# Kernel optimization log

Hardware: AMD Instinct MI355X
Metric: run time of the kernel (lower is better)

## Reference

```python
import jax, jax.numpy as jnp
import numpy as np
from jax import lax

B_, L_, D_ = 4, 3136, 256
DH, DS, DR = 256, 16, 16  # d_inner//2, d_state, dt_rank (ceil(256/16))


def _ln(x, g, b):
    m = x.mean(-1, keepdims=True)
    v = ((x - m) ** 2).mean(-1, keepdims=True)
    return (x - m) * lax.rsqrt(v + 1e-5) * g + b


def _dwconv_same(x, w):
    # x: (B, C, L), w: (C, 1, K) depthwise, padding='same', no bias
    return lax.conv_general_dilated(x, w, (1,), 'SAME',
        dimension_numbers=('NCH', 'OIH', 'NCH'), feature_group_count=x.shape[1])


def _selective_scan(u, delta, A, Bm, Cm, Dp, delta_bias):
    # u, delta: (b, d, l); A: (d, n); Bm, Cm: (b, n, l)
    delta = jax.nn.softplus(delta + delta_bias[None, :, None])
    dA = jnp.exp(jnp.einsum('bdl,dn->lbdn', delta, A))          # (l,b,d,n)
    dBu = jnp.einsum('bdl,bnl,bdl->lbdn', delta, Bm, u)          # (l,b,d,n)
    C_l = jnp.transpose(Cm, (2, 0, 1))                           # (l,b,n)
    h0 = jnp.zeros(dA.shape[1:], u.dtype)

    def step(h, inp):
        dA_t, dBu_t, C_t = inp
        h = dA_t * h + dBu_t
        return h, jnp.einsum('bdn,bn->bd', h, C_t)

    _, ys = lax.scan(step, h0, (dA, dBu, C_l))                   # ys: (l,b,d)
    return jnp.transpose(ys, (1, 2, 0)) + u * Dp[None, :, None]


def _mamba(x, in_proj_w, conv_x_w, conv_z_w, x_proj_w, dt_proj_w, dt_proj_b, A_log, Dp, out_proj_w):
    xz = jnp.einsum('bld,ed->bel', x, in_proj_w)                 # (b, 2*DH, l)
    xb, zb = xz[:, :DH], xz[:, DH:]
    xb = jax.nn.silu(_dwconv_same(xb, conv_x_w))
    zb = jax.nn.silu(_dwconv_same(zb, conv_z_w))
    x_dbl = jnp.einsum('bdl,ed->ble', xb, x_proj_w)              # (b, l, DR+2*DS)
    dt, Bm, Cm = x_dbl[..., :DR], x_dbl[..., DR:DR + DS], x_dbl[..., DR + DS:]
    delta = jnp.einsum('blr,dr->bdl', dt, dt_proj_w)             # (b, DH, l)
    Bm = jnp.transpose(Bm, (0, 2, 1))                            # (b, DS, l)
    Cm = jnp.transpose(Cm, (0, 2, 1))
    A = -jnp.exp(A_log)
    y = _selective_scan(xb, delta, A, Bm, Cm, Dp, dt_proj_b)     # (b, DH, l)
    y = jnp.concatenate([y, zb], axis=1)                         # (b, 2*DH, l)
    return jnp.einsum('bel,de->bld', y, out_proj_w)


def _block(x, ln1_g, ln1_b, ln2_g, ln2_b, in_proj_w, conv_x_w, conv_z_w,
           x_proj_w, dt_proj_w, dt_proj_b, A_log, Dp, out_proj_w,
           mlp_w1, mlp_b1, mlp_w2, mlp_b2):
    x = x + _mamba(_ln(x, ln1_g, ln1_b), in_proj_w, conv_x_w, conv_z_w,
                   x_proj_w, dt_proj_w, dt_proj_b, A_log, Dp, out_proj_w)
    h = _ln(x, ln2_g, ln2_b)
    h = jax.nn.gelu(jnp.einsum('bld,hd->blh', h, mlp_w1) + mlp_b1, approximate=False)
    return x + (jnp.einsum('blh,dh->bld', h, mlp_w2) + mlp_b2)


def setup_inputs() -> dict:
    key = jax.random.key(0)
    ks = jax.random.split(key, 12)
    f = lambda k, s, sc=0.02: jax.random.normal(k, s, dtype=jnp.float32) * sc
    dt = jnp.exp(jax.random.uniform(ks[9], (DH,), dtype=jnp.float32)
                 * (np.log(0.1) - np.log(0.001)) + np.log(0.001))
    dt = jnp.clip(dt, 1e-4)
    inv_dt = dt + jnp.log(-jnp.expm1(-dt))
    return {
        'x': jax.random.normal(ks[0], (B_, L_, D_), dtype=jnp.float32),
        'ln1_g': jnp.ones((D_,), jnp.float32), 'ln1_b': jnp.zeros((D_,), jnp.float32),
        'ln2_g': jnp.ones((D_,), jnp.float32), 'ln2_b': jnp.zeros((D_,), jnp.float32),
        'in_proj_w': f(ks[1], (2 * DH, D_)),
        'conv_x_w': f(ks[2], (DH, 1, 3), 0.1),
        'conv_z_w': f(ks[3], (DH, 1, 3), 0.1),
        'x_proj_w': f(ks[4], (DR + 2 * DS, DH)),
        'dt_proj_w': f(ks[5], (DH, DR), DR ** -0.5),
        'dt_proj_b': inv_dt,
        'A_log': jnp.log(jnp.tile(jnp.arange(1, DS + 1, dtype=jnp.float32)[None, :], (DH, 1))),
        'Dp': jnp.ones((DH,), jnp.float32),
        'out_proj_w': f(ks[6], (D_, 2 * DH)),
        'mlp_w1': f(ks[7], (4 * D_, D_)), 'mlp_b1': jnp.zeros((4 * D_,), jnp.float32),
        'mlp_w2': f(ks[8], (D_, 4 * D_)), 'mlp_b2': jnp.zeros((D_,), jnp.float32),
    }


def reference(x, ln1_g, ln1_b, ln2_g, ln2_b, in_proj_w, conv_x_w, conv_z_w,
              x_proj_w, dt_proj_w, dt_proj_b, A_log, Dp, out_proj_w,
              mlp_w1, mlp_b1, mlp_w2, mlp_b2):
    return _block(x, ln1_g, ln1_b, ln2_g, ln2_b, in_proj_w, conv_x_w, conv_z_w,
                  x_proj_w, dt_proj_w, dt_proj_b, A_log, Dp, out_proj_w,
                  mlp_w1, mlp_b1, mlp_w2, mlp_b2)
```

## Files before the change

kernel.cpp:

```cpp
#include <hip/hip_runtime.h>
#include <hip/hip_bf16.h>

#define B_ 4
#define L_ 3136
#define D_ 256
#define NCH 49
#define LCH 64
#define M_ (B_*L_)

__device__ __forceinline__ float bf2f(unsigned short u) {
    union { unsigned int i; float f; } v; v.i = ((unsigned int)u) << 16; return v.f;
}
__device__ __forceinline__ unsigned short f2bs(float f) {
    __hip_bfloat16 h = __float2bfloat16(f);
    return *(unsigned short*)&h;
}
__device__ __forceinline__ float ldw(const void* p, size_t i, bool bf) {
    return bf ? bf2f(((const unsigned short*)p)[i]) : ((const float*)p)[i];
}
__device__ __forceinline__ void cvt4(ushort4 a, float* o) {
    o[0] = bf2f(a.x); o[1] = bf2f(a.y); o[2] = bf2f(a.z); o[3] = bf2f(a.w);
}
__device__ __forceinline__ void cvt8g(const unsigned short* p, bool v, float* o) {
    if (v) {
        ushort4 a = *(const ushort4*)p;
        ushort4 b = *(const ushort4*)(p + 4);
        cvt4(a, o); cvt4(b, o + 4);
    } else {
        #pragma unroll
        for (int i = 0; i < 8; ++i) o[i] = 0.f;
    }
}
__device__ __forceinline__ float dpp_add_xor1(float x) {
    int m = __builtin_amdgcn_update_dpp(0, __float_as_int(x), 0xB1, 0xF, 0xF, true);
    return x + __int_as_float(m);
}
__device__ __forceinline__ float dpp_add_xor2(float x) {
    int m = __builtin_amdgcn_update_dpp(0, __float_as_int(x), 0x4E, 0xF, 0xF, true);
    return x + __int_as_float(m);
}

__global__ __launch_bounds__(256) void detect_kernel(
    const unsigned int* __restrict__ xw, int* __restrict__ flag)
{
    int t = threadIdx.x; int cnt = 0;
    for (int i = t; i < 2048; i += 256) {
        unsigned int lo = xw[i] & 0xFFFFu;
        unsigned int e = (lo >> 7) & 0xFFu;
        if (e >= 0x58u && e <= 0x97u) cnt++;
    }
    #pragma unroll
    for (int o = 32; o > 0; o >>= 1) cnt += __shfl_down(cnt, o);
    __shared__ int sred[4];
    if ((t & 63) == 0) sred[t >> 6] = cnt;
    __syncthreads();
    if (t == 0) flag[0] = (sred[0] + sred[1] + sred[2] + sred[3] > 1024) ? 1 : 0;
}

__global__ __launch_bounds__(256) void ln_kernel(
    const void* __restrict__ xin, int inmode,
    const void* __restrict__ g, const void* __restrict__ bsh,
    unsigned short* __restrict__ out, const int* __restrict__ flagp)
{
    const bool wbf = (*flagp != 0);
    const bool inbf = (inmode < 0) ? wbf : true;
    int row = blockIdx.x * 4 + (threadIdx.x >> 6);
    int lane = threadIdx.x & 63;
    size_t idx = (size_t)row * 256 + lane * 4;
    float v[4];
    if (inbf) {
        ushort4 a = *(const ushort4*)((const unsigned short*)xin + idx);
        cvt4(a, v);
    } else {
        float4 a = *(const float4*)((const float*)xin + idx);
        v[0] = a.x; v[1] = a.y; v[2] = a.z; v[3] = a.w;
    }
    float s = v[0] + v[1] + v[2] + v[3];
    float s2 = v[0]*v[0] + v[1]*v[1] + v[2]*v[2] + v[3]*v[3];
    #pragma unroll
    for (int o = 32; o > 0; o >>= 1) { s += __shfl_xor(s, o); s2 += __shfl_xor(s2, o); }
    float mean = s * (1.f / 256.f);
    float var  = s2 * (1.f / 256.f) - mean * mean;
    float rs = rsqrtf(var + 1e-5f);
    ushort4 o;
    o.x = f2bs((v[0] - mean) * rs * ldw(g, lane*4+0, wbf) + ldw(bsh, lane*4+0, wbf));
    o.y = f2bs((v[1] - mean) * rs * ldw(g, lane*4+1, wbf) + ldw(bsh, lane*4+1, wbf));
    o.z = f2bs((v[2] - mean) * rs * ldw(g, lane*4+2, wbf) + ldw(bsh, lane*4+2, wbf));
    o.w = f2bs((v[3] - mean) * rs * ldw(g, lane*4+3, wbf) + ldw(bsh, lane*4+3, wbf));
    *(ushort4*)(out + idx) = o;
}

enum { EPI_NONE = 0, EPI_SP = 1, EPI_RES = 2, EPI_GELU = 3, EPI_OUT = 4 };

typedef __attribute__((ext_vector_type(8))) short bf16x8;
typedef __attribute__((ext_vector_type(4))) float f32x4;

__device__ __forceinline__ void gload_lds16(const void* g, void* l) {
    __builtin_amdgcn_global_load_lds(
        (const __attribute__((address_space(1))) unsigned int*)g,
        (__attribute__((address_space(3))) unsigned int*)l, 16, 0, 0);
}

template<int EPI>
__global__ __launch_bounds__(256) void mgemm_kernel(
    const unsigned short* __restrict__ A, const unsigned short* __restrict__ A2, int Ksplit,
    const void* __restrict__ W, void* __restrict__ Cout,
    int N, int K, int lda, int ldc,
    const void* __restrict__ bias, const void* __restrict__ resb,
    const unsigned short* __restrict__ resf, const int* __restrict__ flagp)
{
    const bool wbf = (*flagp != 0);
    __shared__ unsigned short As[2][64][64];
    __shared__ unsigned short Ws[2][64][64];
    const int tid = threadIdx.x;

    const int nwg = gridDim.x * gridDim.y;
    int bid = blockIdx.y * gridDim.x + blockIdx.x;
    int wgid = ((nwg & 7) == 0) ? ((bid & 7) * (nwg >> 3) + (bid >> 3)) : bid;
    const int bx = wgid % gridDim.x;
    const int by = wgid / gridDim.x;
    const int bm = by * 64, bn = bx * 64;

    const int l = tid & 63, wid = tid >> 6;
    const int wr = wid >> 1, wc = wid & 1;
    const int lr = l & 15;
    const int lq = l >> 4;
    const int srow = tid >> 3;
    const int sblk = ((tid & 7) ^ (srow & 7)) * 8;
    const int dcol = (tid & 7) * 8;

    f32x4 acc[2][2] = {};
    const int NT = K >> 6;

    auto stage = [&](int buf, int k0s) {
        const unsigned short* Ab; int kc;
        if (k0s < Ksplit) { Ab = A;  kc = k0s; }
        else              { Ab = A2; kc = k0s - Ksplit; }
        gload_lds16(Ab + (size_t)(bm + srow) * lda + kc + sblk,      &As[buf][srow][dcol]);
        gload_lds16(Ab + (size_t)(bm + 32 + srow) * lda + kc + sblk, &As[buf][32 + srow][dcol]);
        if (wbf) {
            const unsigned short* Wb = (const unsigned short*)W;
            gload_lds16(Wb + (size_t)(bn + srow) * K + k0s + sblk,      &Ws[buf][srow][dcol]);
            gload_lds16(Wb + (size_t)(bn + 32 + srow) * K + k0s + sblk, &Ws[buf][32 + srow][dcol]);
        } else {
            const float* Wf = (const float*)W;
            #pragma unroll
            for (int h = 0; h < 2; ++h) {
                int row = h * 32 + srow;
                const float* p = Wf + (size_t)(bn + row) * K + k0s + (tid & 7) * 8;
                float4 w0 = *(const float4*)p;
                float4 w1 = *(const float4*)(p + 4);
                ushort4 o0, o1;
                o0.x = f2bs(w0.x); o0.y = f2bs(w0.y); o0.z = f2bs(w0.z); o0.w = f2bs(w0.w);
                o1.x = f2bs(w1.x); o1.y = f2bs(w1.y); o1.z = f2bs(w1.z); o1.w = f2bs(w1.w);
                *(ushort4*)&Ws[buf][row][sblk]     = o0;
                *(ushort4*)&Ws[buf][row][sblk + 4] = o1;
            }
        }
    };

    stage(0, 0);
    asm volatile("s_waitcnt vmcnt(0)" ::: "memory");
    __syncthreads();

    int cur = 0;
    for (int kt = 0; kt < NT; ++kt) {
        if (kt + 1 < NT) stage(cur ^ 1, (kt + 1) << 6);

        bf16x8 af[2][2], bfr[2][2];
        #pragma unroll
        for (int i = 0; i < 2; ++i) {
            #pragma unroll
            for (int ks = 0; ks < 2; ++ks) {
                int ca = ((ks * 4 + lq) ^ (lr & 7)) * 8;
                af[i][ks]  = *(const bf16x8*)&As[cur][wr * 32 + i * 16 + lr][ca];
                bfr[i][ks] = *(const bf16x8*)&Ws[cur][wc * 32 + i * 16 + lr][ca];
            }
        }
        #pragma unroll
        for (int ks = 0; ks < 2; ++ks)
            #pragma unroll
            for (int i = 0; i < 2; ++i)
                #pragma unroll
                for (int j = 0; j < 2; ++j)
                    acc[i][j] = __builtin_amdgcn_mfma_f32_16x16x32_bf16(af[i][ks], bfr[j][ks], acc[i][j], 0, 0, 0);

        if (kt + 1 < NT) {
            asm volatile("s_waitcnt vmcnt(0)" ::: "memory");
            __syncthreads();
            cur ^= 1;
        }
    }

    #pragma unroll
    for (int i = 0; i < 2; ++i) {
        #pragma unroll
        for (int j = 0; j < 2; ++j) {
            const int col = bn + wc * 32 + j * 16 + lr;
            #pragma unroll
            for (int e = 0; e < 4; ++e) {
                const int row = bm + wr * 32 + i * 16 + lq * 4 + e;
                float t = acc[i][j][e];
                if (EPI == EPI_RES) {
                    t += ldw(resb, (size_t)row * 256 + col, wbf);
                } else if (EPI == EPI_GELU) {
                    t += ldw(bias, col, wbf);
                    t = 0.5f * t * (1.f + erff(t * 0.70710678118654752f));
                } else if (EPI == EPI_OUT) {
                    t += ldw(bias, col, wbf) + bf2f(resf[(size_t)row * 256 + col]);
                }
                if (EPI == EPI_OUT && !wbf) {
                    ((float*)Cout)[(size_t)row * ldc + col] = t;
                } else {
                    ((unsigned short*)Cout)[(size_t)row * ldc + col] = f2bs(t);
                }
            }
        }
    }
}

__global__ __launch_bounds__(256) void xproj_kernel(
    const unsigned short* __restrict__ A, const void* __restrict__ W,
    float* __restrict__ Cout, const int* __restrict__ flagp)
{
    const bool wbf = (*flagp != 0);
    __shared__ unsigned short As[2][64][64];
    __shared__ unsigned short Ws[2][64][64];
    const int tid = threadIdx.x;
    const int bm = blockIdx.y * 64;

    const int l = tid & 63, wid = tid >> 6;
    const int wr = wid >> 1, wc = wid & 1;
    const int lr = l & 15, lq = l >> 4;
    const int srow = tid >> 3;
    const int sblk = ((tid & 7) ^ (srow & 7)) * 8;
    const int dcol = (tid & 7) * 8;

    {
        ushort4 zz4; zz4.x = 0; zz4.y = 0; zz4.z = 0; zz4.w = 0;
        int buf = tid >> 7, rr = 48 + ((tid >> 3) & 15), cc = (tid & 7) * 8;
        *(ushort4*)&Ws[buf][rr][cc] = zz4;
        *(ushort4*)&Ws[buf][rr][cc + 4] = zz4;
    }
    __syncthreads();

    f32x4 acc[2][2] = {};

    auto stage = [&](int buf, int k0s) {
        gload_lds16(A + (size_t)(bm + srow) * 256 + k0s + sblk,      &As[buf][srow][dcol]);
        gload_lds16(A + (size_t)(bm + 32 + srow) * 256 + k0s + sblk, &As[buf][32 + srow][dcol]);
        if (wbf) {
            const unsigned short* Wb = (const unsigned short*)W;
            gload_lds16(Wb + (size_t)srow * 256 + k0s + sblk, &Ws[buf][srow][dcol]);
            if (srow < 16)
                gload_lds16(Wb + (size_t)(32 + srow) * 256 + k0s + sblk, &Ws[buf][32 + srow][dcol]);
        } else {
            const float* Wf = (const float*)W;
            #pragma unroll
            for (int h = 0; h < 2; ++h) {
                int row = h * 32 + srow;
                if (row < 48) {
                    const float* p = Wf + (size_t)row * 256 + k0s + (tid & 7) * 8;
                    float4 w0 = *(const float4*)p;
                    float4 w1 = *(const float4*)(p + 4);
                    ushort4 o0, o1;
                    o0.x = f2bs(w0.x); o0.y = f2bs(w0.y); o0.z = f2bs(w0.z); o0.w = f2bs(w0.w);
                    o1.x = f2bs(w1.x); o1.y = f2bs(w1.y); o1.z = f2bs(w1.z); o1.w = f2bs(w1.w);
                    *(ushort4*)&Ws[buf][row][sblk]     = o0;
                    *(ushort4*)&Ws[buf][row][sblk + 4] = o1;
                }
            }
        }
    };

    stage(0, 0);
    asm volatile("s_waitcnt vmcnt(0)" ::: "memory");
    __syncthreads();

    int cur = 0;
    for (int kt = 0; kt < 4; ++kt) {
        if (kt + 1 < 4) stage(cur ^ 1, (kt + 1) << 6);
        bf16x8 af[2][2], bfr[2][2];
        #pragma unroll
        for (int i = 0; i < 2; ++i) {
            #pragma unroll
            for (int ks = 0; ks < 2; ++ks) {
                int ca = ((ks * 4 + lq) ^ (lr & 7)) * 8;
                af[i][ks]  = *(const bf16x8*)&As[cur][wr * 32 + i * 16 + lr][ca];
                bfr[i][ks] = *(const bf16x8*)&Ws[cur][wc * 32 + i * 16 + lr][ca];
            }
        }
        #pragma unroll
        for (int ks = 0; ks < 2; ++ks)
            #pragma unroll
            for (int i = 0; i < 2; ++i)
                #pragma unroll
                for (int j = 0; j < 2; ++j)
                    acc[i][j] = __builtin_amdgcn_mfma_f32_16x16x32_bf16(af[i][ks], bfr[j][ks], acc[i][j], 0, 0, 0);
        if (kt + 1 < 4) {
            asm volatile("s_waitcnt vmcnt(0)" ::: "memory");
            __syncthreads();
            cur ^= 1;
        }
    }

    #pragma unroll
    for (int i = 0; i < 2; ++i) {
        #pragma unroll
        for (int j = 0; j < 2; ++j) {
            const int col = wc * 32 + j * 16 + lr;
            if (col < 48) {
                #pragma unroll
                for (int e = 0; e < 4; ++e) {
                    const int row = bm + wr * 32 + i * 16 + lq * 4 + e;
                    Cout[(size_t)row * 48 + col] = acc[i][j][e];
                }
            }
        }
    }
}

__global__ __launch_bounds__(256) void dtgemm_kernel(
    const float* __restrict__ Axd, const void* __restrict__ W,
    unsigned short* __restrict__ Cout, const void* __restrict__ bias,
    const int* __restrict__ flagp)
{
    const bool wbf = (*flagp != 0);
    __shared__ unsigned short Ah[64][16];
    __shared__ unsigned short Al[64][16];
    __shared__ unsigned short Wb[64][16];
    const int tid = threadIdx.x;
    const int nwg = gridDim.x * gridDim.y;
    int bid = blockIdx.y * gridDim.x + blockIdx.x;
    int wgid = ((nwg & 7) == 0) ? ((bid & 7) * (nwg >> 3) + (bid >> 3)) : bid;
    const int bx = wgid % gridDim.x, by = wgid / gridDim.x;
    const int bm = by * 64, bn = bx * 64;

    {
        int rr = tid >> 2, cc = (tid & 3) * 4;
        float4 v = *(const float4*)(Axd + (size_t)(bm + rr) * 48 + cc);
        float vv[4] = {v.x, v.y, v.z, v.w};
        ushort4 hi4, lo4;
        unsigned short* hp = (unsigned short*)&hi4;
        unsigned short* lp = (unsigned short*)&lo4;
        #pragma unroll
        for (int j = 0; j < 4; ++j) {
            unsigned short h = f2bs(vv[j]);
            hp[j] = h;
            lp[j] = f2bs(vv[j] - bf2f(h));
        }
        *(ushort4*)&Ah[rr][cc] = hi4;
        *(ushort4*)&Al[rr][cc] = lo4;
        ushort4 wb4;
        unsigned short* wp = (unsigned short*)&wb4;
        if (wbf) {
            wb4 = *(const ushort4*)((const unsigned short*)W + (size_t)(bn + rr) * 16 + cc);
        } else {
            float4 wv = *(const float4*)((const float*)W + (size_t)(bn + rr) * 16 + cc);
            wp[0] = f2bs(wv.x); wp[1] = f2bs(wv.y); wp[2] = f2bs(wv.z); wp[3] = f2bs(wv.w);
        }
        *(ushort4*)&Wb[rr][cc] = wb4;
    }
    __syncthreads();

    const int l = tid & 63, wid = tid >> 6;
    const int wr = wid >> 1, wc = wid & 1;
    const int lr = l & 15, lq = l >> 4;

    f32x4 acc[2][2] = {};
    bf16x8 ah[2], al8[2], wb8[2];
    #pragma unroll
    for (int i = 0; i < 2; ++i) { ah[i] = bf16x8{}; al8[i] = bf16x8{}; wb8[i] = bf16x8{}; }
    if (lq < 2) {
        #pragma unroll
        for (int i = 0; i < 2; ++i) {
            ah[i]  = *(const bf16x8*)&Ah[wr * 32 + i * 16 + lr][lq * 8];
            al8[i] = *(const bf16x8*)&Al[wr * 32 + i * 16 + lr][lq * 8];
            wb8[i] = *(const bf16x8*)&Wb[wc * 32 + i * 16 + lr][lq * 8];
        }
    }
    #pragma unroll
    for (int i = 0; i < 2; ++i)
        #pragma unroll
        for (int j = 0; j < 2; ++j) {
            acc[i][j] = __builtin_amdgcn_mfma_f32_16x16x32_bf16(ah[i],  wb8[j], acc[i][j], 0, 0, 0);
            acc[i][j] = __builtin_amdgcn_mfma_f32_16x16x32_bf16(al8[i], wb8[j], acc[i][j], 0, 0, 0);
        }

    #pragma unroll
    for (int i = 0; i < 2; ++i) {
        #pragma unroll
        for (int j = 0; j < 2; ++j) {
            const int col = bn + wc * 32 + j * 16 + lr;
            #pragma unroll
            for (int e = 0; e < 4; ++e) {
                const int row = bm + wr * 32 + i * 16 + lq * 4 + e;
                float t = acc[i][j][e] + ldw(bias, col, wbf);
                t = (t > 20.f) ? t : log1pf(__expf(t));
                Cout[(size_t)row * 256 + col] = f2bs(t);
            }
        }
    }
}

__global__ __launch_bounds__(256) void conv_silu_kernel(
    const unsigned short* __restrict__ xz,
    const void* __restrict__ wx, const void* __restrict__ wz,
    unsigned short* __restrict__ u, unsigned short* __restrict__ z,
    const int* __restrict__ flagp)
{
    const bool wbf = (*flagp != 0);
    int sub = threadIdx.x >> 5;
    int cb = (threadIdx.x & 31) * 8;
    int bl = blockIdx.x * 8 + sub;
    int l = bl % L_;
    const unsigned short* r = xz + (size_t)bl * 512;
    bool hasm = (l > 0), hasp = (l < L_ - 1);

    float wxa[24], wza[24];
    if (wbf) {
        const unsigned short* px = (const unsigned short*)wx + 3 * cb;
        const unsigned short* pz = (const unsigned short*)wz + 3 * cb;
        #pragma unroll
        for (int t = 0; t < 3; ++t) {
            cvt4(*(const ushort4*)(px + t * 8), &wxa[t * 8]);
            cvt4(*(const ushort4*)(px + t * 8 + 4), &wxa[t * 8 + 4]);
            cvt4(*(const ushort4*)(pz + t * 8), &wza[t * 8]);
            cvt4(*(const ushort4*)(pz + t * 8 + 4), &wza[t * 8 + 4]);
        }
    } else {
        const float* px = (const float*)wx + 3 * cb;
        const float* pz = (const float*)wz + 3 * cb;
        #pragma unroll
        for (int t = 0; t < 6; ++t) {
            *(float4*)&wxa[t * 4] = *(const float4*)(px + t * 4);
            *(float4*)&wza[t * 4] = *(const float4*)(pz + t * 4);
        }
    }

    float xm[8], xc[8], xp[8];
    cvt8g(r + cb - 512, hasm, xm);
    cvt8g(r + cb,       true, xc);
    cvt8g(r + cb + 512, hasp, xp);
    ushort4 o0, o1;
    {
        unsigned short* op = (unsigned short*)&o0;
        unsigned short* op1 = (unsigned short*)&o1;
        #pragma unroll
        for (int j = 0; j < 8; ++j) {
            float v = xm[j] * wxa[3 * j] + xc[j] * wxa[3 * j + 1] + xp[j] * wxa[3 * j + 2];
            v = v / (1.f + __expf(-v));
            if (j < 4) op[j] = f2bs(v); else op1[j - 4] = f2bs(v);
        }
    }
    *(ushort4*)(u + (size_t)bl * 256 + cb) = o0;
    *(ushort4*)(u + (size_t)bl * 256 + cb + 4) = o1;

    cvt8g(r + cb - 256,  hasm, xm);
    cvt8g(r + 256 + cb,  true, xc);
    cvt8g(r + 768 + cb,  hasp, xp);
    {
        unsigned short* op = (unsigned short*)&o0;
        unsigned short* op1 = (unsigned short*)&o1;
        #pragma unroll
        for (int j = 0; j < 8; ++j) {
            float v = xm[j] * wza[3 * j] + xc[j] * wza[3 * j + 1] + xp[j] * wza[3 * j + 2];
            v = v / (1.f + __expf(-v));
            if (j < 4) op[j] = f2bs(v); else op1[j - 4] = f2bs(v);
        }
    }
    *(ushort4*)(z + (size_t)bl * 256 + cb) = o0;
    *(ushort4*)(z + (size_t)bl * 256 + cb + 4) = o1;
}

__global__ __launch_bounds__(256) void scan_a_kernel(
    const unsigned short* __restrict__ delta, const unsigned short* __restrict__ u,
    const float* __restrict__ xdbl, const void* __restrict__ A_log,
    float* __restrict__ hend, float* __restrict__ dsum, const int* __restrict__ flagp)
{
    const bool wbf = (*flagp != 0);
    int blk = blockIdx.x;
    int b = blk / (NCH * 16);
    int rem = blk % (NCH * 16);
    int c = rem / 16, db = rem % 16;

    __shared__ unsigned int sdu[64][16];
    __shared__ float sB[64][16];

    const unsigned short* dp = delta + (size_t)b * L_ * 256;
    const unsigned short* up = u     + (size_t)b * L_ * 256;
    const float* xd = xdbl + (size_t)b * L_ * 48;

    int r = threadIdx.x >> 2, q = (threadIdx.x & 3) * 4;
    int lrow = c * 64 + r;
    {
        ushort4 dv = *(const ushort4*)(dp + (size_t)lrow * 256 + db * 16 + q);
        ushort4 uv = *(const ushort4*)(up + (size_t)lrow * 256 + db * 16 + q);
        uint4 pk;
        pk.x = (unsigned int)dv.x | ((unsigned int)uv.x << 16);
        pk.y = (unsigned int)dv.y | ((unsigned int)uv.y << 16);
        pk.z = (unsigned int)dv.z | ((unsigned int)uv.z << 16);
        pk.w = (unsigned int)dv.w | ((unsigned int)uv.w << 16);
        *(uint4*)&sdu[r][q] = pk;
        *(float4*)&sB[r][q] = *(const float4*)(xd + (size_t)lrow * 48 + 16 + q);
    }
    __syncthreads();

    int g = threadIdx.x >> 4, n = threadIdx.x & 15;
    int d = db * 16 + g;
    float An2 = -__expf(ldw(A_log, d * 16 + n, wbf)) * 1.44269504088896f;
    float h = 0.f, s = 0.f;
    #pragma unroll 8
    for (int t2 = 0; t2 < 64; ++t2) {
        unsigned int du = sdu[t2][g];
        float ds = __uint_as_float(du << 16);
        float ut = __uint_as_float(du & 0xFFFF0000u);
        float Bn = sB[t2][n];
        float e = exp2f(ds * An2);
        h = fmaf(e, h, ds * ut * Bn);
        s += ds;
    }
    size_t pair = (size_t)b * 256 + d;
    hend[(pair * NCH + c) * 16 + n] = h;
    if (n == 0) dsum[pair * NCH + c] = s;
}

__global__ __launch_bounds__(256) void scan_b_kernel(
    const void* __restrict__ A_log, float* __restrict__ hend,
    const float* __restrict__ dsum, const int* __restrict__ flagp)
{
    const bool wbf = (*flagp != 0);
    int gid = blockIdx.x * 256 + threadIdx.x;
    int pair = gid >> 4, n = gid & 15;
    int d = pair & 255;
    float An = -__expf(ldw(A_log, d * 16 + n, wbf));
    float H = 0.f;
    #pragma unroll 7
    for (int c = 0; c < NCH; ++c) {
        size_t idx = ((size_t)pair * NCH + c) * 16 + n;
        float he = hend[idx];
        hend[idx] = H;
        H = __expf(An * dsum[(size_t)pair * NCH + c]) * H + he;
    }
}

__global__ __launch_bounds__(256) void scan_c_kernel(
    const unsigned short* __restrict__ delta, const unsigned short* __restrict__ u,
    const float* __restrict__ xdbl, const void* __restrict__ A_log,
    const void* __restrict__ Dp, const float* __restrict__ hinit,
    unsigned short* __restrict__ y, const int* __restrict__ flagp)
{
    const bool wbf = (*flagp != 0);
    int blk = blockIdx.x;
    int b = blk / (NCH * 16);
    int rem = blk % (NCH * 16);
    int c = rem / 16, db = rem % 16;

    __shared__ unsigned int sdu[64][16];
    __shared__ float sBC[64][16][2];
    __shared__ float syp[64][16][4];
    __shared__ unsigned short sy[64][16];

    const unsigned short* dp = delta + (size_t)b * L_ * 256;
    const unsigned short* up = u     + (size_t)b * L_ * 256;
    const float* xd = xdbl + (size_t)b * L_ * 48;

    int r = threadIdx.x >> 2, q = (threadIdx.x & 3) * 4;
    int lrow = c * 64 + r;
    {
        ushort4 dv = *(const ushort4*)(dp + (size_t)lrow * 256 + db * 16 + q);
        ushort4 uv = *(const ushort4*)(up + (size_t)lrow * 256 + db * 16 + q);
        uint4 pk;
        pk.x = (unsigned int)dv.x | ((unsigned int)uv.x << 16);
        pk.y = (unsigned int)dv.y | ((unsigned int)uv.y << 16);
        pk.z = (unsigned int)dv.z | ((unsigned int)uv.z << 16);
        pk.w = (unsigned int)dv.w | ((unsigned int)uv.w << 16);
        *(uint4*)&sdu[r][q] = pk;
        float4 Bv = *(const float4*)(xd + (size_t)lrow * 48 + 16 + q);
        float4 Cv = *(const float4*)(xd + (size_t)lrow * 48 + 32 + q);
        float2 p0; p0.x = Bv.x; p0.y = Cv.x; *(float2*)&sBC[r][q + 0][0] = p0;
        float2 p1; p1.x = Bv.y; p1.y = Cv.y; *(float2*)&sBC[r][q + 1][0] = p1;
        float2 p2; p2.x = Bv.z; p2.y = Cv.z; *(float2*)&sBC[r][q + 2][0] = p2;
        float2 p3; p3.x = Bv.w; p3.y = Cv.w; *(float2*)&sBC[r][q + 3][0] = p3;
    }
    __syncthreads();

    int g = threadIdx.x >> 4, n = threadIdx.x & 15;
    int d = db * 16 + g;
    float An2 = -__expf(ldw(A_log, d * 16 + n, wbf)) * 1.44269504088896f;
    size_t pair = (size_t)b * 256 + d;
    float h = hinit[(pair * NCH + c) * 16 + n];
    const bool wlane = ((n & 3) == 0);
    #pragma unroll 4
    for (int t2 = 0; t2 < 64; ++t2) {
        unsigned int du = sdu[t2][g];
        float ds = __uint_as_float(du << 16);
        float ut = __uint_as_float(du & 0xFFFF0000u);
        float2 bc = *(const float2*)&sBC[t2][n][0];
        float e = exp2f(ds * An2);
        h = fmaf(e, h, ds * ut * bc.x);
        float yp = h * bc.y;
        yp = dpp_add_xor1(yp);
        yp = dpp_add_xor2(yp);
        if (wlane) syp[t2][g][n >> 2] = yp;
    }
    __syncthreads();

    #pragma unroll
    for (int cc = 0; cc < 4; ++cc) {
        int cell = threadIdx.x + cc * 256;
        int t2 = cell >> 4, gg = cell & 15;
        float4 p = *(const float4*)&syp[t2][gg][0];
        unsigned int du = sdu[t2][gg];
        float ut = __uint_as_float(du & 0xFFFF0000u);
        float Dd = ldw(Dp, db * 16 + gg, wbf);
        sy[t2][gg] = f2bs(p.x + p.y + p.z + p.w + ut * Dd);
    }
    __syncthreads();
    *(ushort4*)(y + ((size_t)b * L_ + c * 64 + r) * 256 + db * 16 + q) = *(ushort4*)&sy[r][q];
}

extern "C" void kernel_launch(void* const* d_in, const int* in_sizes, int n_in,
                              void* d_out, int out_size, void* d_ws, size_t ws_size,
                              hipStream_t stream) {
    const void* x         = d_in[0];
    const void* ln1_g     = d_in[1];
    const void* ln1_b     = d_in[2];
    const void* ln2_g     = d_in[3];
    const void* ln2_b     = d_in[4];
    const void* in_proj_w = d_in[5];
    const void* conv_x_w  = d_in[6];
    const void* conv_z_w  = d_in[7];
    const void* x_proj_w  = d_in[8];
    const void* dt_proj_w = d_in[9];
    const void* dt_proj_b = d_in[10];
    const void* A_log     = d_in[11];
    const void* Dp        = d_in[12];
    const void* out_proj_w= d_in[13];
    const void* mlp_w1    = d_in[14];
    const void* mlp_b1    = d_in[15];
    const void* mlp_w2    = d_in[16];
    const void* mlp_b2    = d_in[17];

    float* ws = (float*)d_ws;
    unsigned short* xz    = (unsigned short*)(ws);
    unsigned short* delta = (unsigned short*)(ws);
    unsigned short* yb    = (unsigned short*)(ws + 1605632);
    float*          xdbl  = ws + 3211264;
    float*          hend  = ws + 3813376;
    float*          dsum  = ws + 4616192;
    unsigned short* hmid  = (unsigned short*)(ws);
    unsigned short* ub    = (unsigned short*)(ws + 6422528);
    unsigned short* xres  = (unsigned short*)(ws + 6422528);
    unsigned short* xnb   = (unsigned short*)(ws + 8028160);
    int*            flag  = (int*)(ws + 9633792);

    dim3 blk(256);
    const int KNOSPLIT = 1 << 30;

    detect_kernel<<<1, blk, 0, stream>>>((const unsigned int*)x, flag);

    ln_kernel<<<M_ / 4, blk, 0, stream>>>(x, -1, ln1_g, ln1_b, xnb, flag);

    mgemm_kernel<EPI_NONE><<<dim3(8, 196), blk, 0, stream>>>(
        xnb, nullptr, KNOSPLIT, in_proj_w, xz, 512, 256, 256, 512, nullptr, nullptr, nullptr, flag);

    conv_silu_kernel<<<M_ / 8, blk, 0, stream>>>(xz, conv_x_w, conv_z_w, ub, xnb, flag);

    xproj_kernel<<<dim3(1, 196), blk, 0, stream>>>(ub, x_proj_w, xdbl, flag);

    dtgemm_kernel<<<dim3(4, 196), blk, 0, stream>>>(xdbl, dt_proj_w, delta, dt_proj_b, flag);

    scan_a_kernel<<<B_ * NCH * 16, blk, 0, stream>>>(delta, ub, xdbl, A_log, hend, dsum, flag);
    scan_b_kernel<<<64, blk, 0, stream>>>(A_log, hend, dsum, flag);
    scan_c_kernel<<<B_ * NCH * 16, blk, 0, stream>>>(delta, ub, xdbl, A_log, Dp, hend, yb, flag);

    mgemm_kernel<EPI_RES><<<dim3(4, 196), blk, 0, stream>>>(
        yb, xnb, 256, out_proj_w, xres, 256, 512, 256, 256, nullptr, x, nullptr, flag);

    ln_kernel<<<M_ / 4, blk, 0, stream>>>(xres, 1, ln2_g, ln2_b, xnb, flag);

    mgemm_kernel<EPI_GELU><<<dim3(16, 196), blk, 0, stream>>>(
        xnb, nullptr, KNOSPLIT, mlp_w1, hmid, 1024, 256, 256, 1024, mlp_b1, nullptr, nullptr, flag);

    mgemm_kernel<EPI_OUT><<<dim3(4, 196), blk, 0, stream>>>(
        hmid, nullptr, KNOSPLIT, mlp_w2, d_out, 256, 1024, 1024, 256, mlp_b2, nullptr, xres, flag);
}
```

Baseline: 297.2 us.

## Fuse LayerNorm into following GEMMs, merge x_proj with dt_proj, transpose scan LDS

Both LayerNorms are now computed inside a new lngemm kernel that normalizes a 64-row tile into LDS and then runs the MFMA GEMM, so the two standalone LN kernels and their normalized-activation round trips are removed. The x_proj and dt_proj GEMMs are merged into one kernel that keeps the hi/lo split of dt in LDS. The scan kernels switch to transposed LDS layouts for vectorized per-4-timestep reads. In exchange, each N-tile block recomputes LayerNorm for its rows (8x and 16x redundant), and the fused kernel uses more registers and LDS.

```diff
diff --git a/kernel.cpp b/kernel.cpp
--- a/kernel.cpp
+++ b/kernel.cpp
@@ -55,39 +55,6 @@
     if ((t & 63) == 0) sred[t >> 6] = cnt;
     __syncthreads();
     if (t == 0) flag[0] = (sred[0] + sred[1] + sred[2] + sred[3] > 1024) ? 1 : 0;
-}
-
-__global__ __launch_bounds__(256) void ln_kernel(
-    const void* __restrict__ xin, int inmode,
-    const void* __restrict__ g, const void* __restrict__ bsh,
-    unsigned short* __restrict__ out, const int* __restrict__ flagp)
-{
-    const bool wbf = (*flagp != 0);
-    const bool inbf = (inmode < 0) ? wbf : true;
-    int row = blockIdx.x * 4 + (threadIdx.x >> 6);
-    int lane = threadIdx.x & 63;
-    size_t idx = (size_t)row * 256 + lane * 4;
-    float v[4];
-    if (inbf) {
-        ushort4 a = *(const ushort4*)((const unsigned short*)xin + idx);
-        cvt4(a, v);
-    } else {
-        float4 a = *(const float4*)((const float*)xin + idx);
-        v[0] = a.x; v[1] = a.y; v[2] = a.z; v[3] = a.w;
-    }
-    float s = v[0] + v[1] + v[2] + v[3];
-    float s2 = v[0]*v[0] + v[1]*v[1] + v[2]*v[2] + v[3]*v[3];
-    #pragma unroll
-    for (int o = 32; o > 0; o >>= 1) { s += __shfl_xor(s, o); s2 += __shfl_xor(s2, o); }
-    float mean = s * (1.f / 256.f);
-    float var  = s2 * (1.f / 256.f) - mean * mean;
-    float rs = rsqrtf(var + 1e-5f);
-    ushort4 o;
-    o.x = f2bs((v[0] - mean) * rs * ldw(g, lane*4+0, wbf) + ldw(bsh, lane*4+0, wbf));
-    o.y = f2bs((v[1] - mean) * rs * ldw(g, lane*4+1, wbf) + ldw(bsh, lane*4+1, wbf));
-    o.z = f2bs((v[2] - mean) * rs * ldw(g, lane*4+2, wbf) + ldw(bsh, lane*4+2, wbf));
-    o.w = f2bs((v[3] - mean) * rs * ldw(g, lane*4+3, wbf) + ldw(bsh, lane*4+3, wbf));
-    *(ushort4*)(out + idx) = o;
 }
 
 enum { EPI_NONE = 0, EPI_SP = 1, EPI_RES = 2, EPI_GELU = 3, EPI_OUT = 4 };
@@ -203,9 +170,6 @@
                 float t = acc[i][j][e];
                 if (EPI == EPI_RES) {
                     t += ldw(resb, (size_t)row * 256 + col, wbf);
-                } else if (EPI == EPI_GELU) {
-                    t += ldw(bias, col, wbf);
-                    t = 0.5f * t * (1.f + erff(t * 0.70710678118654752f));
                 } else if (EPI == EPI_OUT) {
                     t += ldw(bias, col, wbf) + bf2f(resf[(size_t)row * 256 + col]);
                 }
@@ -219,15 +183,27 @@
     }
 }
 
-__global__ __launch_bounds__(256) void xproj_kernel(
-    const unsigned short* __restrict__ A, const void* __restrict__ W,
-    float* __restrict__ Cout, const int* __restrict__ flagp)
+template<int EPI>
+__global__ __launch_bounds__(256) void lngemm_kernel(
+    const void* __restrict__ Xsrc, int inmode,
+    const void* __restrict__ g, const void* __restrict__ bsh,
+    const void* __restrict__ W, void* __restrict__ Cout,
+    int N, int ldc, const void* __restrict__ bias,
+    const int* __restrict__ flagp)
 {
     const bool wbf = (*flagp != 0);
-    __shared__ unsigned short As[2][64][64];
+    const bool inbf = (inmode < 0) ? wbf : true;
+    __shared__ unsigned short As4[4][64][64];
     __shared__ unsigned short Ws[2][64][64];
     const int tid = threadIdx.x;
-    const int bm = blockIdx.y * 64;
+    const int K = 256;
+
+    const int nwg = gridDim.x * gridDim.y;
+    int bid = blockIdx.y * gridDim.x + blockIdx.x;
+    int wgid = ((nwg & 7) == 0) ? ((bid & 7) * (nwg >> 3) + (bid >> 3)) : bid;
+    const int bx = wgid % gridDim.x;
+    const int by = wgid / gridDim.x;
+    const int bm = by * 64, bn = bx * 64;
 
     const int l = tid & 63, wid = tid >> 6;
     const int wr = wid >> 1, wc = wid & 1;
@@ -236,6 +212,154 @@
     const int sblk = ((tid & 7) ^ (srow & 7)) * 8;
     const int dcol = (tid & 7) * 8;
 
+    auto stageW = [&](int buf, int k0s) {
+        if (wbf) {
+            const unsigned short* Wb = (const unsigned short*)W;
+            gload_lds16(Wb + (size_t)(bn + srow) * K + k0s + sblk,      &Ws[buf][srow][dcol]);
+            gload_lds16(Wb + (size_t)(bn + 32 + srow) * K + k0s + sblk, &Ws[buf][32 + srow][dcol]);
+        } else {
+            const float* Wf = (const float*)W;
+            #pragma unroll
+            for (int h = 0; h < 2; ++h) {
+                int row = h * 32 + srow;
+                const float* p = Wf + (size_t)(bn + row) * K + k0s + (tid & 7) * 8;
+                float4 w0 = *(const float4*)p;
+                float4 w1 = *(const float4*)(p + 4);
+                ushort4 o0, o1;
+                o0.x = f2bs(w0.x); o0.y = f2bs(w0.y); o0.z = f2bs(w0.z); o0.w = f2bs(w0.w);
+                o1.x = f2bs(w1.x); o1.y = f2bs(w1.y); o1.z = f2bs(w1.z); o1.w = f2bs(w1.w);
+                *(ushort4*)&Ws[buf][row][sblk]     = o0;
+                *(ushort4*)&Ws[buf][row][sblk + 4] = o1;
+            }
+        }
+    };
+
+    stageW(0, 0);
+
+    {
+        int r = tid >> 2;
+        int cq = (tid & 3) * 64;
+        float vals[64];
+        const size_t base = (size_t)(bm + r) * 256 + cq;
+        if (inbf) {
+            const unsigned short* xp = (const unsigned short*)Xsrc + base;
+            #pragma unroll
+            for (int jb = 0; jb < 8; ++jb) {
+                cvt4(*(const ushort4*)(xp + jb * 8),     &vals[jb * 8]);
+                cvt4(*(const ushort4*)(xp + jb * 8 + 4), &vals[jb * 8 + 4]);
+            }
+        } else {
+            const float* xp = (const float*)Xsrc + base;
+            #pragma unroll
+            for (int jb = 0; jb < 16; ++jb)
+                *(float4*)&vals[jb * 4] = *(const float4*)(xp + jb * 4);
+        }
+        float s = 0.f, s2 = 0.f;
+        #pragma unroll
+        for (int j2 = 0; j2 < 64; ++j2) { s += vals[j2]; s2 += vals[j2] * vals[j2]; }
+        s  = dpp_add_xor2(dpp_add_xor1(s));
+        s2 = dpp_add_xor2(dpp_add_xor1(s2));
+        float mean = s * (1.f / 256.f);
+        float var  = s2 * (1.f / 256.f) - mean * mean;
+        float rs = rsqrtf(var + 1e-5f);
+        const int kt = tid & 3;
+        #pragma unroll
+        for (int jb = 0; jb < 8; ++jb) {
+            float gv[8], bv[8];
+            if (wbf) {
+                const unsigned short* gp = (const unsigned short*)g + cq + jb * 8;
+                const unsigned short* bp = (const unsigned short*)bsh + cq + jb * 8;
+                cvt4(*(const ushort4*)gp, gv);       cvt4(*(const ushort4*)(gp + 4), gv + 4);
+                cvt4(*(const ushort4*)bp, bv);       cvt4(*(const ushort4*)(bp + 4), bv + 4);
+            } else {
+                const float* gp = (const float*)g + cq + jb * 8;
+                const float* bp = (const float*)bsh + cq + jb * 8;
+                *(float4*)&gv[0] = *(const float4*)gp;     *(float4*)&gv[4] = *(const float4*)(gp + 4);
+                *(float4*)&bv[0] = *(const float4*)bp;     *(float4*)&bv[4] = *(const float4*)(bp + 4);
+            }
+            ushort4 o0, o1;
+            unsigned short* op0 = (unsigned short*)&o0;
+            unsigned short* op1 = (unsigned short*)&o1;
+            #pragma unroll
+            for (int j = 0; j < 8; ++j) {
+                float t = (vals[jb * 8 + j] - mean) * rs * gv[j] + bv[j];
+                if (j < 4) op0[j] = f2bs(t); else op1[j - 4] = f2bs(t);
+            }
+            int wcol = (jb ^ (r & 7)) * 8;
+            *(ushort4*)&As4[kt][r][wcol]     = o0;
+            *(ushort4*)&As4[kt][r][wcol + 4] = o1;
+        }
+    }
+    asm volatile("s_waitcnt vmcnt(0)" ::: "memory");
+    __syncthreads();
+
+    f32x4 acc[2][2] = {};
+    int cur = 0;
+    for (int kt = 0; kt < 4; ++kt) {
+        if (kt + 1 < 4) stageW(cur ^ 1, (kt + 1) << 6);
+        bf16x8 af[2][2], bfr[2][2];
+        #pragma unroll
+        for (int i = 0; i < 2; ++i) {
+            #pragma unroll
+            for (int ks = 0; ks < 2; ++ks) {
+                int ca = ((ks * 4 + lq) ^ (lr & 7)) * 8;
+                af[i][ks]  = *(const bf16x8*)&As4[kt][wr * 32 + i * 16 + lr][ca];
+                bfr[i][ks] = *(const bf16x8*)&Ws[cur][wc * 32 + i * 16 + lr][ca];
+            }
+        }
+        #pragma unroll
+        for (int ks = 0; ks < 2; ++ks)
+            #pragma unroll
+            for (int i = 0; i < 2; ++i)
+                #pragma unroll
+                for (int j = 0; j < 2; ++j)
+                    acc[i][j] = __builtin_amdgcn_mfma_f32_16x16x32_bf16(af[i][ks], bfr[j][ks], acc[i][j], 0, 0, 0);
+        if (kt + 1 < 4) {
+            asm volatile("s_waitcnt vmcnt(0)" ::: "memory");
+            __syncthreads();
+            cur ^= 1;
+        }
+    }
+
+    #pragma unroll
+    for (int i = 0; i < 2; ++i) {
+        #pragma unroll
+        for (int j = 0; j < 2; ++j) {
+            const int col = bn + wc * 32 + j * 16 + lr;
+            #pragma unroll
+            for (int e = 0; e < 4; ++e) {
+                const int row = bm + wr * 32 + i * 16 + lq * 4 + e;
+                float t = acc[i][j][e];
+                if (EPI == EPI_GELU) {
+                    t += ldw(bias, col, wbf);
+                    t = 0.5f * t * (1.f + erff(t * 0.70710678118654752f));
+                }
+                ((unsigned short*)Cout)[(size_t)row * ldc + col] = f2bs(t);
+            }
+        }
+    }
+}
+
+__global__ __launch_bounds__(256) void xdt_kernel(
+    const unsigned short* __restrict__ A, const void* __restrict__ Wx,
+    const void* __restrict__ Wd, float* __restrict__ xdbl,
+    unsigned short* __restrict__ delta, const void* __restrict__ bias,
+    const int* __restrict__ flagp)
+{
+    const bool wbf = (*flagp != 0);
+    __shared__ unsigned short As[2][64][64];
+    __shared__ unsigned short Ws[2][64][64];
+    __shared__ unsigned short Ahl[64][40];
+    const int tid = threadIdx.x;
+    const int bm = blockIdx.y * 64;
+
+    const int l = tid & 63, wid = tid >> 6;
+    const int wr = wid >> 1, wc = wid & 1;
+    const int lr = l & 15, lq = l >> 4;
+    const int srow = tid >> 3;
+    const int sblk = ((tid & 7) ^ (srow & 7)) * 8;
+    const int dcol = (tid & 7) * 8;
+
     {
         ushort4 zz4; zz4.x = 0; zz4.y = 0; zz4.z = 0; zz4.w = 0;
         int buf = tid >> 7, rr = 48 + ((tid >> 3) & 15), cc = (tid & 7) * 8;
@@ -250,12 +374,12 @@
         gload_lds16(A + (size_t)(bm + srow) * 256 + k0s + sblk,      &As[buf][srow][dcol]);
         gload_lds16(A + (size_t)(bm + 32 + srow) * 256 + k0s + sblk, &As[buf][32 + srow][dcol]);
         if (wbf) {
-            const unsigned short* Wb = (const unsigned short*)W;
+            const unsigned short* Wb = (const unsigned short*)Wx;
             gload_lds16(Wb + (size_t)srow * 256 + k0s + sblk, &Ws[buf][srow][dcol]);
             if (srow < 16)
                 gload_lds16(Wb + (size_t)(32 + srow) * 256 + k0s + sblk, &Ws[buf][32 + srow][dcol]);
         } else {
-            const float* Wf = (const float*)W;
+            const float* Wf = (const float*)Wx;
             #pragma unroll
             for (int h = 0; h < 2; ++h) {
                 int row = h * 32 + srow;
@@ -309,95 +433,62 @@
         #pragma unroll
         for (int j = 0; j < 2; ++j) {
             const int col = wc * 32 + j * 16 + lr;
-            if (col < 48) {
-                #pragma unroll
-                for (int e = 0; e < 4; ++e) {
-                    const int row = bm + wr * 32 + i * 16 + lq * 4 + e;
-                    Cout[(size_t)row * 48 + col] = acc[i][j][e];
+            #pragma unroll
+            for (int e = 0; e < 4; ++e) {
+                const int row = wr * 32 + i * 16 + lq * 4 + e;
+                float t = acc[i][j][e];
+                if (col < 48) xdbl[(size_t)(bm + row) * 48 + col] = t;
+                if (wc == 0 && j == 0) {
+                    unsigned short hi = f2bs(t);
+                    Ahl[row][lr]      = hi;
+                    Ahl[row][16 + lr] = f2bs(t - bf2f(hi));
                 }
             }
         }
     }
-}
-
-__global__ __launch_bounds__(256) void dtgemm_kernel(
-    const float* __restrict__ Axd, const void* __restrict__ W,
-    unsigned short* __restrict__ Cout, const void* __restrict__ bias,
-    const int* __restrict__ flagp)
-{
-    const bool wbf = (*flagp != 0);
-    __shared__ unsigned short Ah[64][16];
-    __shared__ unsigned short Al[64][16];
-    __shared__ unsigned short Wb[64][16];
-    const int tid = threadIdx.x;
-    const int nwg = gridDim.x * gridDim.y;
-    int bid = blockIdx.y * gridDim.x + blockIdx.x;
-    int wgid = ((nwg & 7) == 0) ? ((bid & 7) * (nwg >> 3) + (bid >> 3)) : bid;
-    const int bx = wgid % gridDim.x, by = wgid / gridDim.x;
-    const int bm = by * 64, bn = bx * 64;
-
-    {
-        int rr = tid >> 2, cc = (tid & 3) * 4;
-        float4 v = *(const float4*)(Axd + (size_t)(bm + rr) * 48 + cc);
-        float vv[4] = {v.x, v.y, v.z, v.w};
-        ushort4 hi4, lo4;
-        unsigned short* hp = (unsigned short*)&hi4;
-        unsigned short* lp = (unsigned short*)&lo4;
+    __syncthreads();
+
+    const int wcol = wid * 64;
+    const int kc = (lq & 1) * 8;
+    bf16x8 bf[4];
+    #pragma unroll
+    for (int j = 0; j < 4; ++j) {
+        int nrow = wcol + j * 16 + lr;
+        if (wbf) {
+            bf[j] = *(const bf16x8*)((const unsigned short*)Wd + (size_t)nrow * 16 + kc);
+        } else {
+            const float* p = (const float*)Wd + (size_t)nrow * 16 + kc;
+            float4 w0 = *(const float4*)p;
+            float4 w1 = *(const float4*)(p + 4);
+            union { bf16x8 v; unsigned short s[8]; } u8;
+            u8.s[0] = f2bs(w0.x); u8.s[1] = f2bs(w0.y); u8.s[2] = f2bs(w0.z); u8.s[3] = f2bs(w0.w);
+            u8.s[4] = f2bs(w1.x); u8.s[5] = f2bs(w1.y); u8.s[6] = f2bs(w1.z); u8.s[7] = f2bs(w1.w);
+            bf[j] = u8.v;
+        }
+    }
+    bf16x8 af2[4];
+    #pragma unroll
+    for (int i = 0; i < 4; ++i)
+        af2[i] = *(const bf16x8*)&Ahl[i * 16 + lr][lq * 8];
+
+    f32x4 acc2[4][4] = {};
+    #pragma unroll
+    for (int i = 0; i < 4; ++i)
+        #pragma unroll
+        for (int j = 0; j < 4; ++j)
+            acc2[i][j] = __builtin_amdgcn_mfma_f32_16x16x32_bf16(af2[i], bf[j], acc2[i][j], 0, 0, 0);
+
+    #pragma unroll
+    for (int i = 0; i < 4; ++i) {
         #pragma unroll
         for (int j = 0; j < 4; ++j) {
-            unsigned short h = f2bs(vv[j]);
-            hp[j] = h;
-            lp[j] = f2bs(vv[j] - bf2f(h));
-        }
-        *(ushort4*)&Ah[rr][cc] = hi4;
-        *(ushort4*)&Al[rr][cc] = lo4;
-        ushort4 wb4;
-        unsigned short* wp = (unsigned short*)&wb4;
-        if (wbf) {
-            wb4 = *(const ushort4*)((const unsigned short*)W + (size_t)(bn + rr) * 16 + cc);
-        } else {
-            float4 wv = *(const float4*)((const float*)W + (size_t)(bn + rr) * 16 + cc);
-            wp[0] = f2bs(wv.x); wp[1] = f2bs(wv.y); wp[2] = f2bs(wv.z); wp[3] = f2bs(wv.w);
-        }
-        *(ushort4*)&Wb[rr][cc] = wb4;
-    }
-    __syncthreads();
-
-    const int l = tid & 63, wid = tid >> 6;
-    const int wr = wid >> 1, wc = wid & 1;
-    const int lr = l & 15, lq = l >> 4;
-
-    f32x4 acc[2][2] = {};
-    bf16x8 ah[2], al8[2], wb8[2];
-    #pragma unroll
-    for (int i = 0; i < 2; ++i) { ah[i] = bf16x8{}; al8[i] = bf16x8{}; wb8[i] = bf16x8{}; }
-    if (lq < 2) {
-        #pragma unroll
-        for (int i = 0; i < 2; ++i) {
-            ah[i]  = *(const bf16x8*)&Ah[wr * 32 + i * 16 + lr][lq * 8];
-            al8[i] = *(const bf16x8*)&Al[wr * 32 + i * 16 + lr][lq * 8];
-            wb8[i] = *(const bf16x8*)&Wb[wc * 32 + i * 16 + lr][lq * 8];
-        }
-    }
-    #pragma unroll
-    for (int i = 0; i < 2; ++i)
-        #pragma unroll
-        for (int j = 0; j < 2; ++j) {
-            acc[i][j] = __builtin_amdgcn_mfma_f32_16x16x32_bf16(ah[i],  wb8[j], acc[i][j], 0, 0, 0);
-            acc[i][j] = __builtin_amdgcn_mfma_f32_16x16x32_bf16(al8[i], wb8[j], acc[i][j], 0, 0, 0);
-        }
-
-    #pragma unroll
-    for (int i = 0; i < 2; ++i) {
-        #pragma unroll
-        for (int j = 0; j < 2; ++j) {
-            const int col = bn + wc * 32 + j * 16 + lr;
+            const int col = wcol + j * 16 + lr;
             #pragma unroll
             for (int e = 0; e < 4; ++e) {
-                const int row = bm + wr * 32 + i * 16 + lq * 4 + e;
-                float t = acc[i][j][e] + ldw(bias, col, wbf);
+                const int row = i * 16 + lq * 4 + e;
+                float t = acc2[i][j][e] + ldw(bias, col, wbf);
                 t = (t > 20.f) ? t : log1pf(__expf(t));
-                Cout[(size_t)row * 256 + col] = f2bs(t);
+                delta[(size_t)(bm + row) * 256 + col] = f2bs(t);
             }
         }
     }
@@ -484,8 +575,8 @@
     int rem = blk % (NCH * 16);
     int c = rem / 16, db = rem % 16;
 
-    __shared__ unsigned int sdu[64][16];
-    __shared__ float sB[64][16];
+    __shared__ unsigned int sduT[16][68];
+    __shared__ float sBT[16][68];
 
     const unsigned short* dp = delta + (size_t)b * L_ * 256;
     const unsigned short* up = u     + (size_t)b * L_ * 256;
@@ -496,13 +587,13 @@
     {
         ushort4 dv = *(const ushort4*)(dp + (size_t)lrow * 256 + db * 16 + q);
         ushort4 uv = *(const ushort4*)(up + (size_t)lrow * 256 + db * 16 + q);
-        uint4 pk;
-        pk.x = (unsigned int)dv.x | ((unsigned int)uv.x << 16);
-        pk.y = (unsigned int)dv.y | ((unsigned int)uv.y << 16);
-        pk.z = (unsigned int)dv.z | ((unsigned int)uv.z << 16);
-        pk.w = (unsigned int)dv.w | ((unsigned int)uv.w << 16);
-        *(uint4*)&sdu[r][q] = pk;
-        *(float4*)&sB[r][q] = *(const float4*)(xd + (size_t)lrow * 48 + 16 + q);
+        sduT[q + 0][r] = (unsigned)dv.x | ((unsigned)uv.x << 16);
+        sduT[q + 1][r] = (unsigned)dv.y | ((unsigned)uv.y << 16);
+        sduT[q + 2][r] = (unsigned)dv.z | ((unsigned)uv.z << 16);
+        sduT[q + 3][r] = (unsigned)dv.w | ((unsigned)uv.w << 16);
+        float4 Bv = *(const float4*)(xd + (size_t)lrow * 48 + 16 + q);
+        sBT[q + 0][r] = Bv.x; sBT[q + 1][r] = Bv.y;
+        sBT[q + 2][r] = Bv.z; sBT[q + 3][r] = Bv.w;
     }
     __syncthreads();
 
@@ -510,15 +601,20 @@
     int d = db * 16 + g;
     float An2 = -__expf(ldw(A_log, d * 16 + n, wbf)) * 1.44269504088896f;
     float h = 0.f, s = 0.f;
-    #pragma unroll 8
-    for (int t2 = 0; t2 < 64; ++t2) {
-        unsigned int du = sdu[t2][g];
-        float ds = __uint_as_float(du << 16);
-        float ut = __uint_as_float(du & 0xFFFF0000u);
-        float Bn = sB[t2][n];
-        float e = exp2f(ds * An2);
-        h = fmaf(e, h, ds * ut * Bn);
-        s += ds;
+    #pragma unroll 4
+    for (int tb = 0; tb < 16; ++tb) {
+        uint4 du4 = *(const uint4*)&sduT[g][tb * 4];
+        float4 B4 = *(const float4*)&sBT[n][tb * 4];
+        #pragma unroll
+        for (int j = 0; j < 4; ++j) {
+            unsigned du = (j == 0) ? du4.x : (j == 1) ? du4.y : (j == 2) ? du4.z : du4.w;
+            float Bn = (j == 0) ? B4.x : (j == 1) ? B4.y : (j == 2) ? B4.z : B4.w;
+            float ds = __uint_as_float(du << 16);
+            float ut = __uint_as_float(du & 0xFFFF0000u);
+            float e = exp2f(ds * An2);
+            h = fmaf(e, h, ds * ut * Bn);
+            s += ds;
+        }
     }
     size_t pair = (size_t)b * 256 + d;
     hend[(pair * NCH + c) * 16 + n] = h;
@@ -556,9 +652,9 @@
     int rem = blk % (NCH * 16);
     int c = rem / 16, db = rem % 16;
 
-    __shared__ unsigned int sdu[64][16];
-    __shared__ float sBC[64][16][2];
-    __shared__ float syp[64][16][4];
+    __shared__ unsigned int sduT[16][68];
+    __shared__ float sBCT[16][132];
+    __shared__ float sypT[16][4][68];
     __shared__ unsigned short sy[64][16];
 
     const unsigned short* dp = delta + (size_t)b * L_ * 256;
@@ -570,18 +666,16 @@
     {
         ushort4 dv = *(const ushort4*)(dp + (size_t)lrow * 256 + db * 16 + q);
         ushort4 uv = *(const ushort4*)(up + (size_t)lrow * 256 + db * 16 + q);
-        uint4 pk;
-        pk.x = (unsigned int)dv.x | ((unsigned int)uv.x << 16);
-        pk.y = (unsigned int)dv.y | ((unsigned int)uv.y << 16);
-        pk.z = (unsigned int)dv.z | ((unsigned int)uv.z << 16);
-        pk.w = (unsigned int)dv.w | ((unsigned int)uv.w << 16);
-        *(uint4*)&sdu[r][q] = pk;
+        sduT[q + 0][r] = (unsigned)dv.x | ((unsigned)uv.x << 16);
+        sduT[q + 1][r] = (unsigned)dv.y | ((unsigned)uv.y << 16);
+        sduT[q + 2][r] = (unsigned)dv.z | ((unsigned)uv.z << 16);
+        sduT[q + 3][r] = (unsigned)dv.w | ((unsigned)uv.w << 16);
         float4 Bv = *(const float4*)(xd + (size_t)lrow * 48 + 16 + q);
         float4 Cv = *(const float4*)(xd + (size_t)lrow * 48 + 32 + q);
-        float2 p0; p0.x = Bv.x; p0.y = Cv.x; *(float2*)&sBC[r][q + 0][0] = p0;
-        float2 p1; p1.x = Bv.y; p1.y = Cv.y; *(float2*)&sBC[r][q + 1][0] = p1;
-        float2 p2; p2.x = Bv.z; p2.y = Cv.z; *(float2*)&sBC[r][q + 2][0] = p2;
-        float2 p3; p3.x = Bv.w; p3.y = Cv.w; *(float2*)&sBC[r][q + 3][0] = p3;
+        float2 t0; t0.x = Bv.x; t0.y = Cv.x; *(float2*)&sBCT[q + 0][r * 2] = t0;
+        float2 t1; t1.x = Bv.y; t1.y = Cv.y; *(float2*)&sBCT[q + 1][r * 2] = t1;
+        float2 t2; t2.x = Bv.z; t2.y = Cv.z; *(float2*)&sBCT[q + 2][r * 2] = t2;
+        float2 t3; t3.x = Bv.w; t3.y = Cv.w; *(float2*)&sBCT[q + 3][r * 2] = t3;
     }
     __syncthreads();
 
@@ -591,18 +685,28 @@
     size_t pair = (size_t)b * 256 + d;
     float h = hinit[(pair * NCH + c) * 16 + n];
     const bool wlane = ((n & 3) == 0);
+    const int p = n >> 2;
     #pragma unroll 4
-    for (int t2 = 0; t2 < 64; ++t2) {
-        unsigned int du = sdu[t2][g];
-        float ds = __uint_as_float(du << 16);
-        float ut = __uint_as_float(du & 0xFFFF0000u);
-        float2 bc = *(const float2*)&sBC[t2][n][0];
-        float e = exp2f(ds * An2);
-        h = fmaf(e, h, ds * ut * bc.x);
-        float yp = h * bc.y;
-        yp = dpp_add_xor1(yp);
-        yp = dpp_add_xor2(yp);
-        if (wlane) syp[t2][g][n >> 2] = yp;
+    for (int tb = 0; tb < 16; ++tb) {
+        uint4 du4 = *(const uint4*)&sduT[g][tb * 4];
+        float4 bc01 = *(const float4*)&sBCT[n][tb * 8];
+        float4 bc23 = *(const float4*)&sBCT[n][tb * 8 + 4];
+        float yp4[4];
+        #pragma unroll
+        for (int j = 0; j < 4; ++j) {
+            unsigned du = (j == 0) ? du4.x : (j == 1) ? du4.y : (j == 2) ? du4.z : du4.w;
+            float Bn = (j == 0) ? bc01.x : (j == 1) ? bc01.z : (j == 2) ? bc23.x : bc23.z;
+            float Cn = (j == 0) ? bc01.y : (j == 1) ? bc01.w : (j == 2) ? bc23.y : bc23.w;
+            float ds = __uint_as_float(du << 16);
+            float ut = __uint_as_float(du & 0xFFFF0000u);
+            float e = exp2f(ds * An2);
+            h = fmaf(e, h, ds * ut * Bn);
+            float yp = h * Cn;
+            yp = dpp_add_xor1(yp);
+            yp = dpp_add_xor2(yp);
+            yp4[j] = yp;
+        }
+        if (wlane) *(float4*)&sypT[g][p][tb * 4] = *(float4*)yp4;
     }
     __syncthreads();
 
@@ -610,11 +714,11 @@
     for (int cc = 0; cc < 4; ++cc) {
         int cell = threadIdx.x + cc * 256;
         int t2 = cell >> 4, gg = cell & 15;
-        float4 p = *(const float4*)&syp[t2][gg][0];
-        unsigned int du = sdu[t2][gg];
+        float sum = sypT[gg][0][t2] + sypT[gg][1][t2] + sypT[gg][2][t2] + sypT[gg][3][t2];
+        unsigned du = sduT[gg][t2];
         float ut = __uint_as_float(du & 0xFFFF0000u);
         float Dd = ldw(Dp, db * 16 + gg, wbf);
-        sy[t2][gg] = f2bs(p.x + p.y + p.z + p.w + ut * Dd);
+        sy[t2][gg] = f2bs(sum + ut * Dd);
     }
     __syncthreads();
     *(ushort4*)(y + ((size_t)b * L_ + c * 64 + r) * 256 + db * 16 + q) = *(ushort4*)&sy[r][q];
@@ -660,16 +764,13 @@
 
     detect_kernel<<<1, blk, 0, stream>>>((const unsigned int*)x, flag);
 
-    ln_kernel<<<M_ / 4, blk, 0, stream>>>(x, -1, ln1_g, ln1_b, xnb, flag);
-
-    mgemm_kernel<EPI_NONE><<<dim3(8, 196), blk, 0, stream>>>(
-        xnb, nullptr, KNOSPLIT, in_proj_w, xz, 512, 256, 256, 512, nullptr, nullptr, nullptr, flag);
+    lngemm_kernel<EPI_NONE><<<dim3(8, 196), blk, 0, stream>>>(
+        x, -1, ln1_g, ln1_b, in_proj_w, xz, 512, 512, nullptr, flag);
 
     conv_silu_kernel<<<M_ / 8, blk, 0, stream>>>(xz, conv_x_w, conv_z_w, ub, xnb, flag);
 
-    xproj_kernel<<<dim3(1, 196), blk, 0, stream>>>(ub, x_proj_w, xdbl, flag);
-
-    dtgemm_kernel<<<dim3(4, 196), blk, 0, stream>>>(xdbl, dt_proj_w, delta, dt_proj_b, flag);
+    xdt_kernel<<<dim3(1, 196), blk, 0, stream>>>(
+        ub, x_proj_w, dt_proj_w, xdbl, delta, dt_proj_b, flag);
 
     scan_a_kernel<<<B_ * NCH * 16, blk, 0, stream>>>(delta, ub, xdbl, A_log, hend, dsum, flag);
     scan_b_kernel<<<64, blk, 0, stream>>>(A_log, hend, dsum, flag);
@@ -678,10 +779,8 @@
     mgemm_kernel<EPI_RES><<<dim3(4, 196), blk, 0, stream>>>(
         yb, xnb, 256, out_proj_w, xres, 256, 512, 256, 256, nullptr, x, nullptr, flag);
 
-    ln_kernel<<<M_ / 4, blk, 0, stream>>>(xres, 1, ln2_g, ln2_b, xnb, flag);
-
-    mgemm_kernel<EPI_GELU><<<dim3(16, 196), blk, 0, stream>>>(
-        xnb, nullptr, KNOSPLIT, mlp_w1, hmid, 1024, 256, 256, 1024, mlp_b1, nullptr, nullptr, flag);
+    lngemm_kernel<EPI_GELU><<<dim3(16, 196), blk, 0, stream>>>(
+        xres, 1, ln2_g, ln2_b, mlp_w1, hmid, 1024, 1024, mlp_b1, flag);
 
     mgemm_kernel<EPI_OUT><<<dim3(4, 196), blk, 0, stream>>>(
         hmid, nullptr, KNOSPLIT, mlp_w2, d_out, 256, 1024, 1024, 256, mlp_b2, nullptr, xres, flag);
```

After: 382.0 us. +28.5%, slower.
